# Kernel optimization log

Hardware: AMD Instinct MI355X
Metric: run time of the kernel (lower is better)

## Reference

```python
import jax, jax.numpy as jnp
import numpy as np

S, B, D, H, DH, E, F = 2048, 2, 512, 8, 64, 8, 1024
TOPK = 2


def setup_inputs() -> dict:
    key = jax.random.key(0)
    ks = jax.random.split(key, 12)
    rn = lambda k, shp, s=0.02: jax.random.normal(k, shp, jnp.float32) * s
    # RoPE tables (half-split convention): (S, DH)
    pos = jnp.arange(S, dtype=jnp.float32)[:, None]
    inv_freq = 1.0 / (10000.0 ** (jnp.arange(0, DH, 2, dtype=jnp.float32) / DH))
    ang = pos * inv_freq[None, :]                       # (S, DH//2)
    cos = jnp.concatenate([jnp.cos(ang), jnp.cos(ang)], axis=-1)
    sin = jnp.concatenate([jnp.sin(ang), jnp.sin(ang)], axis=-1)
    return {
        "src": jax.random.normal(ks[0], (S, B, D), jnp.float32),
        "cos": cos, "sin": sin,
        "Wq": rn(ks[1], (D, D)), "bq": jnp.zeros((D,), jnp.float32),
        "Wk": rn(ks[2], (D, D)), "bk": jnp.zeros((D,), jnp.float32),
        "Wv": rn(ks[3], (D, D)), "bv": jnp.zeros((D,), jnp.float32),
        "Wo": rn(ks[4], (D, D)), "bo": jnp.zeros((D,), jnp.float32),
        "ln1_g": jnp.ones((D,), jnp.float32), "ln1_b": jnp.zeros((D,), jnp.float32),
        "ln2_g": jnp.ones((D,), jnp.float32), "ln2_b": jnp.zeros((D,), jnp.float32),
        "Wg": rn(ks[5], (D, E)),
        "W1": rn(ks[6], (E, D, F)), "B1": jnp.zeros((E, F), jnp.float32),
        "W2": rn(ks[7], (E, F, D)), "B2": jnp.zeros((E, D), jnp.float32),
    }


def _layernorm(x, g, b, eps=1e-5):
    m = x.mean(-1, keepdims=True)
    v = ((x - m) ** 2).mean(-1, keepdims=True)
    return (x - m) * jax.lax.rsqrt(v + eps) * g + b


def _rotate_half(x):
    x1, x2 = jnp.split(x, 2, axis=-1)
    return jnp.concatenate([-x2, x1], axis=-1)


def _forward(src, cos, sin, Wq, bq, Wk, bk, Wv, bv, Wo, bo,
             ln1_g, ln1_b, ln2_g, ln2_b, Wg, W1, B1, W2, B2):
    # ---- RoPE self-attention ----
    q = (src @ Wq + bq).reshape(S, B, H, DH)
    k = (src @ Wk + bk).reshape(S, B, H, DH)
    v = (src @ Wv + bv).reshape(S, B, H, DH)
    c = cos[:, None, None, :]
    s = sin[:, None, None, :]
    q = q * c + _rotate_half(q) * s
    k = k * c + _rotate_half(k) * s
    scores = jnp.einsum("sbhd,tbhd->bhst", q, k) / jnp.sqrt(jnp.float32(DH))
    attn = jax.nn.softmax(scores, axis=-1)              # (B,H,S,S)
    ctx = jnp.einsum("bhst,tbhd->sbhd", attn, v).reshape(S, B, D)
    attn_out = ctx @ Wo + bo
    x = _layernorm(src + attn_out, ln1_g, ln1_b)
    # ---- MoE feed-forward (top-k softmax gating) ----
    xt = x.reshape(S * B, D)                            # (N, D)
    probs = jax.nn.softmax(xt @ Wg, axis=-1)            # (N, E)
    top_v, top_i = jax.lax.top_k(probs, TOPK)           # (N, TOPK)
    top_v = top_v / top_v.sum(-1, keepdims=True)
    N = S * B
    gates = jnp.zeros((N, E), jnp.float32).at[
        jnp.arange(N)[:, None], top_i].add(top_v)       # (N, E)
    h = jax.nn.relu(jnp.einsum("nd,edf->nef", xt, W1) + B1[None])   # (N,E,F)
    eo = jnp.einsum("nef,efd->ned", h, W2) + B2[None]               # (N,E,D)
    moe_out = jnp.einsum("ne,ned->nd", gates, eo).reshape(S, B, D)
    return _layernorm(x + moe_out, ln2_g, ln2_b)


def reference(src, cos, sin, Wq, bq, Wk, bk, Wv, bv, Wo, bo,
              ln1_g, ln1_b, ln2_g, ln2_b, Wg, W1, B1, W2, B2):
    return _forward(src, cos, sin, Wq, bq, Wk, bk, Wv, bv, Wo, bo,
                    ln1_g, ln1_b, ln2_g, ln2_b, Wg, W1, B1, W2, B2)
```

## Files before the change

kernel.cpp:

```cpp
#include <hip/hip_runtime.h>
#include <math.h>

#define S_  2048
#define B_  2
#define D_  512
#define H_  8
#define DH_ 64
#define E_  8
#define F_  1024
#define N_  4096
#define NPAIR_ 8192

typedef __attribute__((ext_vector_type(4))) float f32x4;
typedef __attribute__((ext_vector_type(8))) short short8;
typedef unsigned short u16;

__device__ __forceinline__ u16 f2bf(float f) {
  unsigned u = __builtin_bit_cast(unsigned, f);
  u += 0x7fffu + ((u >> 16) & 1u);
  return (u16)(u >> 16);
}
__device__ __forceinline__ float bf2f(u16 h) {
  unsigned u = ((unsigned)h) << 16;
  return __builtin_bit_cast(float, u);
}

__global__ __launch_bounds__(256) void src_split(const float* __restrict__ in,
                                                 u16* __restrict__ hi,
                                                 u16* __restrict__ lo) {
  size_t i = ((size_t)blockIdx.x * 256 + threadIdx.x) * 8;
  float f[8];
  *(float4*)&f[0] = *(const float4*)&in[i];
  *(float4*)&f[4] = *(const float4*)&in[i + 4];
  short8 h, l;
#pragma unroll
  for (int j = 0; j < 8; ++j) {
    u16 a = f2bf(f[j]);
    h[j] = (short)a;
    l[j] = (short)f2bf(f[j] - bf2f(a));
  }
  *(short8*)&hi[i] = h;
  *(short8*)&lo[i] = l;
}

__global__ __launch_bounds__(256) void wsplit_t(const float* __restrict__ W,
                                                u16* __restrict__ Whi,
                                                u16* __restrict__ Wlo,
                                                int Nn, int K) {
  __shared__ u16 Th[64][72];
  __shared__ u16 Tl[64][72];
  int kb = blockIdx.y * 64, nb = blockIdx.x * 64;
  int r = threadIdx.x >> 2, c0 = (threadIdx.x & 3) * 16;
  const float* wp = &W[(size_t)(kb + r) * Nn + nb + c0];
#pragma unroll
  for (int c = 0; c < 16; c += 4) {
    float4 t = *(const float4*)&wp[c];
    float f[4] = {t.x, t.y, t.z, t.w};
#pragma unroll
    for (int j = 0; j < 4; ++j) {
      u16 a = f2bf(f[j]);
      Th[r][c0 + c + j] = a;
      Tl[r][c0 + c + j] = f2bf(f[j] - bf2f(a));
    }
  }
  __syncthreads();
  short8 h0, h1, l0, l1;
#pragma unroll
  for (int j = 0; j < 8; ++j) {
    h0[j] = (short)Th[c0 + j][r];     h1[j] = (short)Th[c0 + 8 + j][r];
    l0[j] = (short)Tl[c0 + j][r];     l1[j] = (short)Tl[c0 + 8 + j][r];
  }
  size_t ob = (size_t)(nb + r) * K + kb + c0;
  *(short8*)&Whi[ob] = h0;  *(short8*)&Whi[ob + 8] = h1;
  *(short8*)&Wlo[ob] = l0;  *(short8*)&Wlo[ob + 8] = l1;
}

__global__ __launch_bounds__(256) void wtrans(const float* __restrict__ W,
                                              u16* __restrict__ Wt,
                                              int K, int Nn) {
  size_t eo = (size_t)blockIdx.z * K * Nn;
  __shared__ u16 T[64][72];
  int kb = blockIdx.y * 64, nb = blockIdx.x * 64;
  int r = threadIdx.x >> 2, c0 = (threadIdx.x & 3) * 16;
  const float* wp = &W[eo + (size_t)(kb + r) * Nn + nb + c0];
#pragma unroll
  for (int c = 0; c < 16; c += 4) {
    float4 t = *(const float4*)&wp[c];
    T[r][c0 + c + 0] = f2bf(t.x);
    T[r][c0 + c + 1] = f2bf(t.y);
    T[r][c0 + c + 2] = f2bf(t.z);
    T[r][c0 + c + 3] = f2bf(t.w);
  }
  __syncthreads();
  short8 s0, s1;
#pragma unroll
  for (int j = 0; j < 8; ++j) {
    s0[j] = (short)T[c0 + j][r];
    s1[j] = (short)T[c0 + 8 + j][r];
  }
  *(short8*)&Wt[eo + (size_t)(nb + r) * K + kb + c0] = s0;
  *(short8*)&Wt[eo + (size_t)(nb + r) * K + kb + c0 + 8] = s1;
}

__global__ __launch_bounds__(256) void qkv_mfma(const u16* __restrict__ Ah_g,
                                                const u16* __restrict__ Al_g,
                                                const u16* __restrict__ Bh_g,
                                                const u16* __restrict__ Bl_g,
                                                const float* __restrict__ bq,
                                                const float* __restrict__ bk,
                                                const float* __restrict__ bv,
                                                const float* __restrict__ cosb,
                                                const float* __restrict__ sinb,
                                                u16* __restrict__ qh, u16* __restrict__ ql,
                                                u16* __restrict__ kh, u16* __restrict__ kl,
                                                u16* __restrict__ vb) {
  __shared__ u16 Ah[128][40], Al[128][40], Bh[128][40], Bl[128][40];
  int tid = threadIdx.x;
  int w = tid >> 6, l = tid & 63;
  int wr = w >> 1, wc = w & 1;
  int lg = l >> 4, lx = l & 15;
  int m0 = blockIdx.x * 128, n0 = blockIdx.y * 128;
  int sr = tid >> 1, s16 = (tid & 1) * 16;
  const u16* Aph = Ah_g + (size_t)(m0 + sr) * 512;
  const u16* Apl = Al_g + (size_t)(m0 + sr) * 512;
  const u16* Bph = Bh_g + (size_t)(n0 + sr) * 512;
  const u16* Bpl = Bl_g + (size_t)(n0 + sr) * 512;
  f32x4 acc[4][4];
#pragma unroll
  for (int m = 0; m < 4; ++m)
#pragma unroll
    for (int n = 0; n < 4; ++n) acc[m][n] = (f32x4){0.f, 0.f, 0.f, 0.f};
  for (int k0 = 0; k0 < 512; k0 += 32) {
    short8 ah0 = *(const short8*)&Aph[k0 + s16];
    short8 ah1 = *(const short8*)&Aph[k0 + s16 + 8];
    short8 al0 = *(const short8*)&Apl[k0 + s16];
    short8 al1 = *(const short8*)&Apl[k0 + s16 + 8];
    short8 bh0 = *(const short8*)&Bph[k0 + s16];
    short8 bh1 = *(const short8*)&Bph[k0 + s16 + 8];
    short8 bl0 = *(const short8*)&Bpl[k0 + s16];
    short8 bl1 = *(const short8*)&Bpl[k0 + s16 + 8];
    __syncthreads();
    *(short8*)&Ah[sr][s16] = ah0; *(short8*)&Ah[sr][s16 + 8] = ah1;
    *(short8*)&Al[sr][s16] = al0; *(short8*)&Al[sr][s16 + 8] = al1;
    *(short8*)&Bh[sr][s16] = bh0; *(short8*)&Bh[sr][s16 + 8] = bh1;
    *(short8*)&Bl[sr][s16] = bl0; *(short8*)&Bl[sr][s16 + 8] = bl1;
    __syncthreads();
    short8 fah[4], fal[4], fbh[4], fbl[4];
#pragma unroll
    for (int m = 0; m < 4; ++m) {
      fah[m] = *(const short8*)&Ah[wr * 64 + m * 16 + lx][lg * 8];
      fal[m] = *(const short8*)&Al[wr * 64 + m * 16 + lx][lg * 8];
    }
#pragma unroll
    for (int n = 0; n < 4; ++n) {
      fbh[n] = *(const short8*)&Bh[wc * 64 + n * 16 + lx][lg * 8];
      fbl[n] = *(const short8*)&Bl[wc * 64 + n * 16 + lx][lg * 8];
    }
#pragma unroll
    for (int m = 0; m < 4; ++m)
#pragma unroll
      for (int n = 0; n < 4; ++n) {
        acc[m][n] = __builtin_amdgcn_mfma_f32_16x16x32_bf16(fah[m], fbh[n], acc[m][n], 0, 0, 0);
        acc[m][n] = __builtin_amdgcn_mfma_f32_16x16x32_bf16(fal[m], fbh[n], acc[m][n], 0, 0, 0);
        acc[m][n] = __builtin_amdgcn_mfma_f32_16x16x32_bf16(fah[m], fbl[n], acc[m][n], 0, 0, 0);
      }
  }
  int tcolbase = n0 + wc * 64;
  int tsel = tcolbase >> 9;
  int hbase = tcolbase & 511;
  const float* bias = (tsel == 0) ? bq : (tsel == 1) ? bk : bv;
  if (tsel == 2) {
#pragma unroll
    for (int m = 0; m < 4; ++m)
#pragma unroll
      for (int i = 0; i < 4; ++i) {
        int row = m0 + wr * 64 + m * 16 + lg * 4 + i;
#pragma unroll
        for (int n = 0; n < 4; ++n) {
          int col = hbase + n * 16 + lx;
          vb[(size_t)row * 512 + col] = f2bf(acc[m][n][i] + bias[col]);
        }
      }
  } else {
    u16* oh = tsel ? kh : qh;
    u16* ol = tsel ? kl : ql;
    float qsc = tsel ? 1.f : 0.125f;
#pragma unroll
    for (int m = 0; m < 4; ++m)
#pragma unroll
      for (int i = 0; i < 4; ++i) {
        int row = m0 + wr * 64 + m * 16 + lg * 4 + i;
        int s = row >> 1;
#pragma unroll
        for (int n = 0; n < 2; ++n) {
          int dln = n * 16 + lx;
          float c  = cosb[s * 64 + dln];
          float sn = sinb[s * 64 + dln];
          float a  = acc[m][n][i]     + bias[hbase + dln];
          float b2 = acc[m][n + 2][i] + bias[hbase + dln + 32];
          float ra = (a * c - b2 * sn) * qsc;
          float rb = (b2 * c + a * sn) * qsc;
          size_t ix = (size_t)row * 512 + hbase + dln;
          u16 rah = f2bf(ra);
          oh[ix] = rah; ol[ix] = f2bf(ra - bf2f(rah));
          u16 rbh = f2bf(rb);
          oh[ix + 32] = rbh; ol[ix + 32] = f2bf(rb - bf2f(rbh));
        }
      }
  }
}

__global__ __launch_bounds__(256) void attn_mfma2(const u16* __restrict__ qh,
                                                  const u16* __restrict__ ql,
                                                  const u16* __restrict__ kh,
                                                  const u16* __restrict__ kl,
                                                  const u16* __restrict__ vbuf,
                                                  u16* __restrict__ poh,
                                                  u16* __restrict__ pol,
                                                  float* __restrict__ pml) {
  __shared__ u16 Khi[64][72];
  __shared__ u16 Klo[64][72];
  __shared__ u16 Vt[64][72];
  __shared__ u16 Pl[4][16][72];
  int tid = threadIdx.x;
  int w = tid >> 6, l = tid & 63;
  int lg = l >> 4, lx = l & 15;
  int f = blockIdx.x;
  int xcd = f & 7, j = f >> 3;
  int slab = xcd + 8 * (j & 3);
  int qt = j >> 2;
  int bh = slab >> 1, kvh = slab & 1;
  int b = bh >> 3, h = bh & 7;

  short8 qfh[2], qfl[2];
  {
    int qrow = qt * 64 + w * 16 + lx;
    size_t qo = (size_t)(qrow * 2 + b) * 512 + h * 64 + lg * 8;
    qfh[0] = *(const short8*)&qh[qo];
    qfh[1] = *(const short8*)&qh[qo + 32];
    qfl[0] = *(const short8*)&ql[qo];
    qfl[1] = *(const short8*)&ql[qo + 32];
  }

  f32x4 o_acc[4];
#pragma unroll
  for (int dg = 0; dg < 4; ++dg) o_acc[dg] = (f32x4){0.f, 0.f, 0.f, 0.f};
  float m_run[4], l_run[4];
#pragma unroll
  for (int i = 0; i < 4; ++i) { m_run[i] = -1e30f; l_run[i] = 0.f; }

  int kvr = tid >> 2, ds4 = (tid & 3) * 16;
  int kvc = tid & 63, dsg = (tid >> 6) * 16;

  for (int tt = 0; tt < 1024; tt += 64) {
    int t0 = kvh * 1024 + tt;
    __syncthreads();
    {
      size_t ko = (size_t)((t0 + kvr) * 2 + b) * 512 + h * 64 + ds4;
      *(short8*)&Khi[kvr][ds4]     = *(const short8*)&kh[ko];
      *(short8*)&Khi[kvr][ds4 + 8] = *(const short8*)&kh[ko + 8];
      *(short8*)&Klo[kvr][ds4]     = *(const short8*)&kl[ko];
      *(short8*)&Klo[kvr][ds4 + 8] = *(const short8*)&kl[ko + 8];
      size_t vo = (size_t)((t0 + kvc) * 2 + b) * 512 + h * 64 + dsg;
      short8 v0 = *(const short8*)&vbuf[vo];
      short8 v1 = *(const short8*)&vbuf[vo + 8];
#pragma unroll
      for (int c = 0; c < 8; ++c) {
        Vt[dsg + c][kvc] = (u16)v0[c];
        Vt[dsg + 8 + c][kvc] = (u16)v1[c];
      }
    }
    __syncthreads();

    f32x4 sc[4];
#pragma unroll
    for (int cg = 0; cg < 4; ++cg) {
      short8 kh0 = *(const short8*)&Khi[cg * 16 + lx][lg * 8];
      short8 kh1 = *(const short8*)&Khi[cg * 16 + lx][32 + lg * 8];
      short8 kl0 = *(const short8*)&Klo[cg * 16 + lx][lg * 8];
      short8 kl1 = *(const short8*)&Klo[cg * 16 + lx][32 + lg * 8];
      f32x4 a = (f32x4){0.f, 0.f, 0.f, 0.f};
      a = __builtin_amdgcn_mfma_f32_16x16x32_bf16(qfh[0], kh0, a, 0, 0, 0);
      a = __builtin_amdgcn_mfma_f32_16x16x32_bf16(qfh[1], kh1, a, 0, 0, 0);
      a = __builtin_amdgcn_mfma_f32_16x16x32_bf16(qfl[0], kh0, a, 0, 0, 0);
      a = __builtin_amdgcn_mfma_f32_16x16x32_bf16(qfl[1], kh1, a, 0, 0, 0);
      a = __builtin_amdgcn_mfma_f32_16x16x32_bf16(qfh[0], kl0, a, 0, 0, 0);
      a = __builtin_amdgcn_mfma_f32_16x16x32_bf16(qfh[1], kl1, a, 0, 0, 0);
      sc[cg] = a;
    }

#pragma unroll
    for (int i = 0; i < 4; ++i) {
      float s0 = sc[0][i], s1 = sc[1][i], s2 = sc[2][i], s3 = sc[3][i];
      float tm = fmaxf(fmaxf(s0, s1), fmaxf(s2, s3));
      tm = fmaxf(tm, __shfl_xor(tm, 1));
      tm = fmaxf(tm, __shfl_xor(tm, 2));
      tm = fmaxf(tm, __shfl_xor(tm, 4));
      tm = fmaxf(tm, __shfl_xor(tm, 8));
      float mn = fmaxf(m_run[i], tm);
      float corr = __expf(m_run[i] - mn);
      m_run[i] = mn;
      float p0 = __expf(s0 - mn), p1 = __expf(s1 - mn);
      float p2 = __expf(s2 - mn), p3 = __expf(s3 - mn);
      float ts = p0 + p1 + p2 + p3;
      ts += __shfl_xor(ts, 1); ts += __shfl_xor(ts, 2);
      ts += __shfl_xor(ts, 4); ts += __shfl_xor(ts, 8);
      l_run[i] = l_run[i] * corr + ts;
#pragma unroll
      for (int dg = 0; dg < 4; ++dg) o_acc[dg][i] *= corr;
      int row = lg * 4 + i;
      Pl[w][row][lx]      = f2bf(p0);
      Pl[w][row][16 + lx] = f2bf(p1);
      Pl[w][row][32 + lx] = f2bf(p2);
      Pl[w][row][48 + lx] = f2bf(p3);
    }

    short8 pa0 = *(const short8*)&Pl[w][lx][lg * 8];
    short8 pa1 = *(const short8*)&Pl[w][lx][32 + lg * 8];
#pragma unroll
    for (int dg = 0; dg < 4; ++dg) {
      short8 v0 = *(const short8*)&Vt[dg * 16 + lx][lg * 8];
      short8 v1 = *(const short8*)&Vt[dg * 16 + lx][32 + lg * 8];
      o_acc[dg] = __builtin_amdgcn_mfma_f32_16x16x32_bf16(pa0, v0, o_acc[dg], 0, 0, 0);
      o_acc[dg] = __builtin_amdgcn_mfma_f32_16x16x32_bf16(pa1, v1, o_acc[dg], 0, 0, 0);
    }
  }

#pragma unroll
  for (int i = 0; i < 4; ++i) {
    int srow = qt * 64 + w * 16 + lg * 4 + i;
    int row2 = srow * 2 + b;
    size_t base = (size_t)kvh * ((size_t)N_ * D_) + (size_t)row2 * 512 + h * 64;
#pragma unroll
    for (int dg = 0; dg < 4; ++dg) {
      float val = o_acc[dg][i];
      u16 hi = f2bf(val);
      poh[base + dg * 16 + lx] = hi;
      pol[base + dg * 16 + lx] = f2bf(val - bf2f(hi));
    }
    if (lx == 0) {
      int u = row2 * 8 + h;
      pml[(size_t)kvh * 65536 + u * 2 + 0] = m_run[i];
      pml[(size_t)kvh * 65536 + u * 2 + 1] = l_run[i];
    }
  }
}

__global__ __launch_bounds__(256) void merge_attn2(const u16* __restrict__ poh,
                                                   const u16* __restrict__ pol,
                                                   const float* __restrict__ pml,
                                                   u16* __restrict__ ch,
                                                   u16* __restrict__ cl) {
  int u = blockIdx.x * 4 + (threadIdx.x >> 6);
  int lane = threadIdx.x & 63;
  float m0 = pml[u * 2], l0 = pml[u * 2 + 1];
  float m1 = pml[65536 + u * 2], l1 = pml[65536 + u * 2 + 1];
  float m = fmaxf(m0, m1);
  float e0 = __expf(m0 - m), e1 = __expf(m1 - m);
  float inv = 1.f / (l0 * e0 + l1 * e1);
  int n = u >> 3, h = u & 7;
  size_t base = (size_t)n * 512 + h * 64 + lane;
  const size_t PO1 = (size_t)N_ * D_;
  float v0 = bf2f(poh[base]) + bf2f(pol[base]);
  float v1 = bf2f(poh[PO1 + base]) + bf2f(pol[PO1 + base]);
  float val = (v0 * e0 + v1 * e1) * inv;
  u16 hi = f2bf(val);
  ch[base] = hi;
  cl[base] = f2bf(val - bf2f(hi));
}

__global__ __launch_bounds__(256) void wo_mfma(const u16* __restrict__ Ah_g,
                                               const u16* __restrict__ Al_g,
                                               const u16* __restrict__ Bh_g,
                                               const u16* __restrict__ Bl_g,
                                               const float* __restrict__ bias,
                                               float* __restrict__ C) {
  __shared__ u16 Ah[128][40], Al[128][40], Bh[128][40], Bl[128][40];
  int tid = threadIdx.x;
  int w = tid >> 6, l = tid & 63;
  int wr = w >> 1, wc = w & 1;
  int lg = l >> 4, lx = l & 15;
  int m0 = blockIdx.x * 128, n0 = blockIdx.y * 128;
  int sr = tid >> 1, s16 = (tid & 1) * 16;
  const u16* Aph = Ah_g + (size_t)(m0 + sr) * 512;
  const u16* Apl = Al_g + (size_t)(m0 + sr) * 512;
  const u16* Bph = Bh_g + (size_t)(n0 + sr) * 512;
  const u16* Bpl = Bl_g + (size_t)(n0 + sr) * 512;
  f32x4 acc[4][4];
#pragma unroll
  for (int m = 0; m < 4; ++m)
#pragma unroll
    for (int n = 0; n < 4; ++n) acc[m][n] = (f32x4){0.f, 0.f, 0.f, 0.f};
  for (int k0 = 0; k0 < 512; k0 += 32) {
    short8 ah0 = *(const short8*)&Aph[k0 + s16];
    short8 ah1 = *(const short8*)&Aph[k0 + s16 + 8];
    short8 al0 = *(const short8*)&Apl[k0 + s16];
    short8 al1 = *(const short8*)&Apl[k0 + s16 + 8];
    short8 bh0 = *(const short8*)&Bph[k0 + s16];
    short8 bh1 = *(const short8*)&Bph[k0 + s16 + 8];
    short8 bl0 = *(const short8*)&Bpl[k0 + s16];
    short8 bl1 = *(const short8*)&Bpl[k0 + s16 + 8];
    __syncthreads();
    *(short8*)&Ah[sr][s16] = ah0; *(short8*)&Ah[sr][s16 + 8] = ah1;
    *(short8*)&Al[sr][s16] = al0; *(short8*)&Al[sr][s16 + 8] = al1;
    *(short8*)&Bh[sr][s16] = bh0; *(short8*)&Bh[sr][s16 + 8] = bh1;
    *(short8*)&Bl[sr][s16] = bl0; *(short8*)&Bl[sr][s16 + 8] = bl1;
    __syncthreads();
    short8 fah[4], fal[4], fbh[4], fbl[4];
#pragma unroll
    for (int m = 0; m < 4; ++m) {
      fah[m] = *(const short8*)&Ah[wr * 64 + m * 16 + lx][lg * 8];
      fal[m] = *(const short8*)&Al[wr * 64 + m * 16 + lx][lg * 8];
    }
#pragma unroll
    for (int n = 0; n < 4; ++n) {
      fbh[n] = *(const short8*)&Bh[wc * 64 + n * 16 + lx][lg * 8];
      fbl[n] = *(const short8*)&Bl[wc * 64 + n * 16 + lx][lg * 8];
    }
#pragma unroll
    for (int m = 0; m < 4; ++m)
#pragma unroll
      for (int n = 0; n < 4; ++n) {
        acc[m][n] = __builtin_amdgcn_mfma_f32_16x16x32_bf16(fah[m], fbh[n], acc[m][n], 0, 0, 0);
        acc[m][n] = __builtin_amdgcn_mfma_f32_16x16x32_bf16(fal[m], fbh[n], acc[m][n], 0, 0, 0);
        acc[m][n] = __builtin_amdgcn_mfma_f32_16x16x32_bf16(fah[m], fbl[n], acc[m][n], 0, 0, 0);
      }
  }
#pragma unroll
  for (int m = 0; m < 4; ++m)
#pragma unroll
    for (int i = 0; i < 4; ++i) {
      int row = m0 + wr * 64 + m * 16 + lg * 4 + i;
#pragma unroll
      for (int n = 0; n < 4; ++n) {
        int col = n0 + wc * 64 + n * 16 + lx;
        C[(size_t)row * 512 + col] = acc[m][n][i] + bias[col];
      }
    }
}

__global__ __launch_bounds__(256) void ln_res(const float* __restrict__ a,
                                              const float* __restrict__ b,
                                              const float* __restrict__ g,
                                              const float* __restrict__ beta,
                                              float* __restrict__ out,
                                              u16* __restrict__ obf) {
  int n = blockIdx.x * 4 + (threadIdx.x >> 6);
  int lane = threadIdx.x & 63;
  float v[8];
  float s = 0.f;
#pragma unroll
  for (int i = 0; i < 8; ++i) {
    int d = lane + 64 * i;
    v[i] = a[(size_t)n * D_ + d] + b[(size_t)n * D_ + d];
    s += v[i];
  }
#pragma unroll
  for (int m = 32; m; m >>= 1) s += __shfl_xor(s, m);
  float mean = s * (1.f / D_);
  float s2 = 0.f;
#pragma unroll
  for (int i = 0; i < 8; ++i) { float t = v[i] - mean; s2 += t * t; }
#pragma unroll
  for (int m = 32; m; m >>= 1) s2 += __shfl_xor(s2, m);
  float r = rsqrtf(s2 * (1.f / D_) + 1e-5f);
#pragma unroll
  for (int i = 0; i < 8; ++i) {
    int d = lane + 64 * i;
    float val = (v[i] - mean) * r * g[d] + beta[d];
    out[(size_t)n * D_ + d] = val;
    obf[(size_t)n * D_ + d] = f2bf(val);
  }
}

__global__ __launch_bounds__(256) void ln2_final(const float* __restrict__ x,
                                                 const u16* __restrict__ mp,
                                                 const float* __restrict__ g,
                                                 const float* __restrict__ beta,
                                                 float* __restrict__ out) {
  int n = blockIdx.x * 4 + (threadIdx.x >> 6);
  int lane = threadIdx.x & 63;
  float v[8];
  float s = 0.f;
#pragma unroll
  for (int i = 0; i < 8; ++i) {
    int d = lane + 64 * i;
    v[i] = x[(size_t)n * D_ + d] + bf2f(mp[(size_t)(2 * n) * D_ + d]) +
           bf2f(mp[(size_t)(2 * n + 1) * D_ + d]);
    s += v[i];
  }
#pragma unroll
  for (int m = 32; m; m >>= 1) s += __shfl_xor(s, m);
  float mean = s * (1.f / D_);
  float s2 = 0.f;
#pragma unroll
  for (int i = 0; i < 8; ++i) { float t = v[i] - mean; s2 += t * t; }
#pragma unroll
  for (int m = 32; m; m >>= 1) s2 += __shfl_xor(s2, m);
  float r = rsqrtf(s2 * (1.f / D_) + 1e-5f);
#pragma unroll
  for (int i = 0; i < 8; ++i) {
    int d = lane + 64 * i;
    out[(size_t)n * D_ + d] = (v[i] - mean) * r * g[d] + beta[d];
  }
}

__global__ __launch_bounds__(256) void gate_compute(const float* __restrict__ x,
                                                    const float* __restrict__ Wg,
                                                    float* __restrict__ gp,
                                                    int* __restrict__ tope) {
  int n = blockIdx.x * 4 + (threadIdx.x >> 6);
  int lane = threadIdx.x & 63;
  float p[E_] = {};
  for (int d = lane; d < D_; d += 64) {
    float xv = x[(size_t)n * D_ + d];
    const float* wr = &Wg[(size_t)d * E_];
#pragma unroll
    for (int e = 0; e < E_; ++e) p[e] += xv * wr[e];
  }
#pragma unroll
  for (int e = 0; e < E_; ++e)
#pragma unroll
    for (int m = 32; m; m >>= 1) p[e] += __shfl_xor(p[e], m);
  if (lane == 0) {
    float mx = p[0];
#pragma unroll
    for (int e = 1; e < E_; ++e) mx = fmaxf(mx, p[e]);
    float q[E_];
#pragma unroll
    for (int e = 0; e < E_; ++e) q[e] = expf(p[e] - mx);
    int e1 = 0;
#pragma unroll
    for (int e = 1; e < E_; ++e) if (q[e] > q[e1]) e1 = e;
    int e2 = (e1 == 0) ? 1 : 0;
#pragma unroll
    for (int e = 0; e < E_; ++e) if (e != e1 && q[e] > q[e2]) e2 = e;
    float denom = q[e1] + q[e2];
    gp[n * 2] = q[e1] / denom;
    gp[n * 2 + 1] = q[e2] / denom;
    tope[n] = e1 | (e2 << 8);
  }
}

__global__ __launch_bounds__(256) void route_build(const int* __restrict__ tope,
                                                   int* __restrict__ cnt,
                                                   int* __restrict__ lst) {
  int e = blockIdx.x;
  __shared__ int wsum[4];
  __shared__ int basem;
  int tid = threadIdx.x;
  int w = tid >> 6, lane = tid & 63;
  if (tid == 0) basem = 0;
  __syncthreads();
  for (int c0 = 0; c0 < N_; c0 += 256) {
    int n = c0 + tid;
    int te = tope[n];
    int e1 = te & 0xff, e2 = (te >> 8) & 0xff;
    bool m2 = (e2 == e);
    bool flag = (e1 == e) || m2;
    unsigned long long mask = __ballot(flag);
    int wpre = __popcll(mask & ((1ull << lane) - 1ull));
    if (lane == 0) wsum[w] = __popcll(mask);
    __syncthreads();
    int woff = 0;
    for (int i = 0; i < w; ++i) woff += wsum[i];
    int total = wsum[0] + wsum[1] + wsum[2] + wsum[3];
    if (flag) lst[e * N_ + basem + woff + wpre] = n * 2 + (m2 ? 1 : 0);
    __syncthreads();
    if (tid == 0) basem += total;
    __syncthreads();
  }
  if (tid == 0) cnt[e] = basem;
}

template <int MODE>
__global__ __launch_bounds__(256) void moe_mfma(const u16* __restrict__ Abase,
                                                const u16* __restrict__ Wt,
                                                const float* __restrict__ bias,
                                                const float* __restrict__ gp,
                                                u16* __restrict__ outp,
                                                const int* __restrict__ cnt,
                                                const int* __restrict__ lst) {
  constexpr int K  = MODE ? 1024 : 512;
  constexpr int Nn = MODE ? 512 : 1024;
  constexpr int NT = Nn / 128;
  constexpr int NI = K / 32;
  int fidx = blockIdx.x;
  int e = fidx & 7;
  int r = fidx >> 3;
  int nt = r % NT;
  int mt = r / NT;
  int c = cnt[e];
  int m0 = mt * 64;
  if (m0 >= c) return;
  int off = 0;
#pragma unroll
  for (int i = 0; i < E_; ++i) if (i < e) off += cnt[i];
  int n0 = nt * 128;
  __shared__ u16 As[64][40];
  __shared__ u16 Bs[128][40];
  int tid = threadIdx.x;
  int w = tid >> 6, l = tid & 63;
  int lg = l >> 4, lx = l & 15;
  int arow = tid >> 2, aseg = (tid & 3) * 8;
  int brow = tid >> 1, bseg = (tid & 1) * 16;
  int ar = m0 + arow; if (ar >= c) ar = c - 1;
  const u16* Ap;
  if (MODE == 0) Ap = Abase + (size_t)(lst[e * N_ + ar] >> 1) * 512 + aseg;
  else           Ap = Abase + (size_t)(off + ar) * 1024 + aseg;
  const u16* Bp = Wt + (size_t)e * K * Nn + (size_t)(n0 + brow) * K + bseg;

  f32x4 acc[4][2];
#pragma unroll
  for (int m = 0; m < 4; ++m)
#pragma unroll
    for (int n = 0; n < 2; ++n) acc[m][n] = (f32x4){0.f, 0.f, 0.f, 0.f};

  short8 pa  = *(const short8*)&Ap[0];
  short8 pb0 = *(const short8*)&Bp[0];
  short8 pb1 = *(const short8*)&Bp[8];
  for (int kk = 0; kk < NI; ++kk) {
    __syncthreads();
    *(short8*)&As[arow][aseg] = pa;
    *(short8*)&Bs[brow][bseg] = pb0;
    *(short8*)&Bs[brow][bseg + 8] = pb1;
    __syncthreads();
    if (kk + 1 < NI) {
      int ko = (kk + 1) * 32;
      pa  = *(const short8*)&Ap[ko];
      pb0 = *(const short8*)&Bp[ko];
      pb1 = *(const short8*)&Bp[ko + 8];
    }
    short8 af[4], bf[2];
#pragma unroll
    for (int m = 0; m < 4; ++m)
      af[m] = *(const short8*)&As[m * 16 + lx][lg * 8];
#pragma unroll
    for (int n = 0; n < 2; ++n)
      bf[n] = *(const short8*)&Bs[w * 32 + n * 16 + lx][lg * 8];
#pragma unroll
    for (int m = 0; m < 4; ++m)
#pragma unroll
      for (int n = 0; n < 2; ++n)
        acc[m][n] = __builtin_amdgcn_mfma_f32_16x16x32_bf16(af[m], bf[n], acc[m][n], 0, 0, 0);
  }
#pragma unroll
  for (int m = 0; m < 4; ++m)
#pragma unroll
    for (int i = 0; i < 4; ++i) {
      int rr = m0 + m * 16 + lg * 4 + i;
      if (rr < c) {
#pragma unroll
        for (int n = 0; n < 2; ++n) {
          int col = n0 + w * 32 + n * 16 + lx;
          float val = acc[m][n][i] + bias[e * Nn + col];
          if (MODE == 0) {
            outp[(size_t)(off + rr) * 1024 + col] = f2bf(fmaxf(val, 0.f));
          } else {
            int p = lst[e * N_ + rr];
            outp[(size_t)p * 512 + col] = f2bf(gp[p] * val);
          }
        }
      }
    }
}

extern "C" void kernel_launch(void* const* d_in, const int* in_sizes, int n_in,
                              void* d_out, int out_size, void* d_ws, size_t ws_size,
                              hipStream_t stream) {
  const float* src  = (const float*)d_in[0];
  const float* cosb = (const float*)d_in[1];
  const float* sinb = (const float*)d_in[2];
  const float* Wq   = (const float*)d_in[3];
  const float* bq   = (const float*)d_in[4];
  const float* Wk   = (const float*)d_in[5];
  const float* bk   = (const float*)d_in[6];
  const float* Wv   = (const float*)d_in[7];
  const float* bv   = (const float*)d_in[8];
  const float* Wo   = (const float*)d_in[9];
  const float* bo   = (const float*)d_in[10];
  const float* ln1g = (const float*)d_in[11];
  const float* ln1b = (const float*)d_in[12];
  const float* ln2g = (const float*)d_in[13];
  const float* ln2b = (const float*)d_in[14];
  const float* Wg   = (const float*)d_in[15];
  const float* W1   = (const float*)d_in[16];
  const float* B1   = (const float*)d_in[17];
  const float* W2   = (const float*)d_in[18];
  const float* B2   = (const float*)d_in[19];
  float* out = (float*)d_out;
  char* wsb = (char*)d_ws;

  const size_t MB1 = 1u << 20;
  u16* sh   = (u16*)(wsb + 0 * MB1);
  u16* sl   = (u16*)(wsb + 4 * MB1);
  u16* qhb  = (u16*)(wsb + 8 * MB1);
  u16* qlb  = (u16*)(wsb + 12 * MB1);
  u16* khb  = (u16*)(wsb + 16 * MB1);
  u16* klb  = (u16*)(wsb + 20 * MB1);
  u16* vbuf = (u16*)(wsb + 24 * MB1);
  u16* poh  = (u16*)(wsb + 28 * MB1);
  u16* pol  = (u16*)(wsb + 36 * MB1);
  float* pml = (float*)(wsb + 44 * MB1);
  float* aob = (float*)(wsb + 28 * MB1);
  float* xb  = (float*)(wsb + 36 * MB1);
  u16* xbf   = (u16*)(wsb + 44 * MB1);
  u16* Wqkv_hi = (u16*)(wsb + 48 * MB1);
  u16* Wqkv_lo = (u16*)(wsb + 48 * MB1 + 1572864);
  u16* Wo_hi   = (u16*)(wsb + 48 * MB1 + 3145728);
  u16* Wo_lo   = (u16*)(wsb + 48 * MB1 + 3670016);
  u16* W1t     = (u16*)(wsb + 52 * MB1);
  u16* W2t     = (u16*)(wsb + 28 * MB1);
  float* gpb   = (float*)(wsb + 60 * MB1);
  int* cnt     = (int*)(wsb + 60 * MB1 + 32768);
  int* lst     = (int*)(wsb + 60 * MB1 + 32768 + 64);
  int* tope    = (int*)(wsb + 60 * MB1 + 32768 + 64 + 131072);
  u16* ch  = sh;
  u16* cl  = sl;
  u16* hbf = (u16*)(wsb + 8 * MB1);
  u16* mp  = (u16*)(wsb + 0 * MB1);

  dim3 blk(256);
  src_split<<<dim3(1024), blk, 0, stream>>>(src, sh, sl);
  wsplit_t<<<dim3(8, 8), blk, 0, stream>>>(Wq, Wqkv_hi, Wqkv_lo, 512, 512);
  wsplit_t<<<dim3(8, 8), blk, 0, stream>>>(Wk, Wqkv_hi + 512 * 512, Wqkv_lo + 512 * 512, 512, 512);
  wsplit_t<<<dim3(8, 8), blk, 0, stream>>>(Wv, Wqkv_hi + 1024 * 512, Wqkv_lo + 1024 * 512, 512, 512);
  wsplit_t<<<dim3(8, 8), blk, 0, stream>>>(Wo, Wo_hi, Wo_lo, 512, 512);
  qkv_mfma<<<dim3(32, 12), blk, 0, stream>>>(sh, sl, Wqkv_hi, Wqkv_lo, bq, bk, bv,
                                             cosb, sinb, qhb, qlb, khb, klb, vbuf);
  attn_mfma2<<<dim3(1024), blk, 0, stream>>>(qhb, qlb, khb, klb, vbuf, poh, pol, pml);
  merge_attn2<<<dim3(8192), blk, 0, stream>>>(poh, pol, pml, ch, cl);
  wo_mfma<<<dim3(32, 4), blk, 0, stream>>>(ch, cl, Wo_hi, Wo_lo, bo, aob);
  ln_res<<<dim3(1024), blk, 0, stream>>>(src, aob, ln1g, ln1b, xb, xbf);
  wtrans<<<dim3(8, 16, 8), blk, 0, stream>>>(W2, W2t, 1024, 512);
  wtrans<<<dim3(16, 8, 8), blk, 0, stream>>>(W1, W1t, 512, 1024);
  gate_compute<<<dim3(1024), blk, 0, stream>>>(xb, Wg, gpb, tope);
  route_build<<<dim3(8), blk, 0, stream>>>(tope, cnt, lst);
  moe_mfma<0><<<dim3(8 * 8 * 64), blk, 0, stream>>>(xbf, W1t, B1, gpb, hbf, cnt, lst);
  moe_mfma<1><<<dim3(8 * 4 * 64), blk, 0, stream>>>(hbf, W2t, B2, gpb, mp, cnt, lst);
  ln2_final<<<dim3(1024), blk, 0, stream>>>(xb, mp, ln2g, ln2b, out);
}
```

Before: 253.5 us.

## Prefetch next K-tile into registers in GEMMs and attention, swizzle P buffer

The QKV GEMM, the output GEMM and the flash-attention loop now load the next K/V or A/B tile from global memory into registers right after the LDS store barrier. This lets the global-load latency overlap with the MFMA work on the current tile. The attention P scratch buffer also gets an XOR swizzle on the column index to cut LDS bank conflicts between the P writes and the pa0/pa1 reads. The cost is higher register pressure from the prefetch registers, which could lower occupancy.

```diff
diff --git a/kernel.cpp b/kernel.cpp
--- a/kernel.cpp
+++ b/kernel.cpp
@@ -130,21 +130,28 @@
   for (int m = 0; m < 4; ++m)
 #pragma unroll
     for (int n = 0; n < 4; ++n) acc[m][n] = (f32x4){0.f, 0.f, 0.f, 0.f};
+  short8 ah0 = *(const short8*)&Aph[s16];
+  short8 ah1 = *(const short8*)&Aph[s16 + 8];
+  short8 al0 = *(const short8*)&Apl[s16];
+  short8 al1 = *(const short8*)&Apl[s16 + 8];
+  short8 bh0 = *(const short8*)&Bph[s16];
+  short8 bh1 = *(const short8*)&Bph[s16 + 8];
+  short8 bl0 = *(const short8*)&Bpl[s16];
+  short8 bl1 = *(const short8*)&Bpl[s16 + 8];
   for (int k0 = 0; k0 < 512; k0 += 32) {
-    short8 ah0 = *(const short8*)&Aph[k0 + s16];
-    short8 ah1 = *(const short8*)&Aph[k0 + s16 + 8];
-    short8 al0 = *(const short8*)&Apl[k0 + s16];
-    short8 al1 = *(const short8*)&Apl[k0 + s16 + 8];
-    short8 bh0 = *(const short8*)&Bph[k0 + s16];
-    short8 bh1 = *(const short8*)&Bph[k0 + s16 + 8];
-    short8 bl0 = *(const short8*)&Bpl[k0 + s16];
-    short8 bl1 = *(const short8*)&Bpl[k0 + s16 + 8];
     __syncthreads();
     *(short8*)&Ah[sr][s16] = ah0; *(short8*)&Ah[sr][s16 + 8] = ah1;
     *(short8*)&Al[sr][s16] = al0; *(short8*)&Al[sr][s16 + 8] = al1;
     *(short8*)&Bh[sr][s16] = bh0; *(short8*)&Bh[sr][s16 + 8] = bh1;
     *(short8*)&Bl[sr][s16] = bl0; *(short8*)&Bl[sr][s16 + 8] = bl1;
     __syncthreads();
+    if (k0 + 32 < 512) {
+      int ko = k0 + 32 + s16;
+      ah0 = *(const short8*)&Aph[ko]; ah1 = *(const short8*)&Aph[ko + 8];
+      al0 = *(const short8*)&Apl[ko]; al1 = *(const short8*)&Apl[ko + 8];
+      bh0 = *(const short8*)&Bph[ko]; bh1 = *(const short8*)&Bph[ko + 8];
+      bl0 = *(const short8*)&Bpl[ko]; bl1 = *(const short8*)&Bpl[ko + 8];
+    }
     short8 fah[4], fal[4], fbh[4], fbl[4];
 #pragma unroll
     for (int m = 0; m < 4; ++m) {
@@ -251,41 +258,53 @@
 
   int kvr = tid >> 2, ds4 = (tid & 3) * 16;
   int kvc = tid & 63, dsg = (tid >> 6) * 16;
+  int psw = ((lx >> 2) & 3) << 3;
+
+  short8 rkh0, rkh1, rkl0, rkl1, rv0, rv1;
+  {
+    int t0 = kvh * 1024;
+    size_t ko = (size_t)((t0 + kvr) * 2 + b) * 512 + h * 64 + ds4;
+    rkh0 = *(const short8*)&kh[ko]; rkh1 = *(const short8*)&kh[ko + 8];
+    rkl0 = *(const short8*)&kl[ko]; rkl1 = *(const short8*)&kl[ko + 8];
+    size_t vo = (size_t)((t0 + kvc) * 2 + b) * 512 + h * 64 + dsg;
+    rv0 = *(const short8*)&vbuf[vo]; rv1 = *(const short8*)&vbuf[vo + 8];
+  }
 
   for (int tt = 0; tt < 1024; tt += 64) {
-    int t0 = kvh * 1024 + tt;
-    __syncthreads();
-    {
+    __syncthreads();
+    *(short8*)&Khi[kvr][ds4]     = rkh0;
+    *(short8*)&Khi[kvr][ds4 + 8] = rkh1;
+    *(short8*)&Klo[kvr][ds4]     = rkl0;
+    *(short8*)&Klo[kvr][ds4 + 8] = rkl1;
+#pragma unroll
+    for (int c = 0; c < 8; ++c) {
+      Vt[dsg + c][kvc] = (u16)rv0[c];
+      Vt[dsg + 8 + c][kvc] = (u16)rv1[c];
+    }
+    __syncthreads();
+    if (tt + 64 < 1024) {
+      int t0 = kvh * 1024 + tt + 64;
       size_t ko = (size_t)((t0 + kvr) * 2 + b) * 512 + h * 64 + ds4;
-      *(short8*)&Khi[kvr][ds4]     = *(const short8*)&kh[ko];
-      *(short8*)&Khi[kvr][ds4 + 8] = *(const short8*)&kh[ko + 8];
-      *(short8*)&Klo[kvr][ds4]     = *(const short8*)&kl[ko];
-      *(short8*)&Klo[kvr][ds4 + 8] = *(const short8*)&kl[ko + 8];
+      rkh0 = *(const short8*)&kh[ko]; rkh1 = *(const short8*)&kh[ko + 8];
+      rkl0 = *(const short8*)&kl[ko]; rkl1 = *(const short8*)&kl[ko + 8];
       size_t vo = (size_t)((t0 + kvc) * 2 + b) * 512 + h * 64 + dsg;
-      short8 v0 = *(const short8*)&vbuf[vo];
-      short8 v1 = *(const short8*)&vbuf[vo + 8];
-#pragma unroll
-      for (int c = 0; c < 8; ++c) {
-        Vt[dsg + c][kvc] = (u16)v0[c];
-        Vt[dsg + 8 + c][kvc] = (u16)v1[c];
-      }
-    }
-    __syncthreads();
+      rv0 = *(const short8*)&vbuf[vo]; rv1 = *(const short8*)&vbuf[vo + 8];
+    }
 
     f32x4 sc[4];
 #pragma unroll
     for (int cg = 0; cg < 4; ++cg) {
-      short8 kh0 = *(const short8*)&Khi[cg * 16 + lx][lg * 8];
-      short8 kh1 = *(const short8*)&Khi[cg * 16 + lx][32 + lg * 8];
-      short8 kl0 = *(const short8*)&Klo[cg * 16 + lx][lg * 8];
-      short8 kl1 = *(const short8*)&Klo[cg * 16 + lx][32 + lg * 8];
+      short8 kf0 = *(const short8*)&Khi[cg * 16 + lx][lg * 8];
+      short8 kf1 = *(const short8*)&Khi[cg * 16 + lx][32 + lg * 8];
+      short8 kg0 = *(const short8*)&Klo[cg * 16 + lx][lg * 8];
+      short8 kg1 = *(const short8*)&Klo[cg * 16 + lx][32 + lg * 8];
       f32x4 a = (f32x4){0.f, 0.f, 0.f, 0.f};
-      a = __builtin_amdgcn_mfma_f32_16x16x32_bf16(qfh[0], kh0, a, 0, 0, 0);
-      a = __builtin_amdgcn_mfma_f32_16x16x32_bf16(qfh[1], kh1, a, 0, 0, 0);
-      a = __builtin_amdgcn_mfma_f32_16x16x32_bf16(qfl[0], kh0, a, 0, 0, 0);
-      a = __builtin_amdgcn_mfma_f32_16x16x32_bf16(qfl[1], kh1, a, 0, 0, 0);
-      a = __builtin_amdgcn_mfma_f32_16x16x32_bf16(qfh[0], kl0, a, 0, 0, 0);
-      a = __builtin_amdgcn_mfma_f32_16x16x32_bf16(qfh[1], kl1, a, 0, 0, 0);
+      a = __builtin_amdgcn_mfma_f32_16x16x32_bf16(qfh[0], kf0, a, 0, 0, 0);
+      a = __builtin_amdgcn_mfma_f32_16x16x32_bf16(qfh[1], kf1, a, 0, 0, 0);
+      a = __builtin_amdgcn_mfma_f32_16x16x32_bf16(qfl[0], kf0, a, 0, 0, 0);
+      a = __builtin_amdgcn_mfma_f32_16x16x32_bf16(qfl[1], kf1, a, 0, 0, 0);
+      a = __builtin_amdgcn_mfma_f32_16x16x32_bf16(qfh[0], kg0, a, 0, 0, 0);
+      a = __builtin_amdgcn_mfma_f32_16x16x32_bf16(qfh[1], kg1, a, 0, 0, 0);
       sc[cg] = a;
     }
 
@@ -309,14 +328,15 @@
 #pragma unroll
       for (int dg = 0; dg < 4; ++dg) o_acc[dg][i] *= corr;
       int row = lg * 4 + i;
-      Pl[w][row][lx]      = f2bf(p0);
-      Pl[w][row][16 + lx] = f2bf(p1);
-      Pl[w][row][32 + lx] = f2bf(p2);
-      Pl[w][row][48 + lx] = f2bf(p3);
-    }
-
-    short8 pa0 = *(const short8*)&Pl[w][lx][lg * 8];
-    short8 pa1 = *(const short8*)&Pl[w][lx][32 + lg * 8];
+      int sw = ((row >> 2) & 3) << 3;
+      Pl[w][row][lx ^ sw]        = f2bf(p0);
+      Pl[w][row][(16 + lx) ^ sw] = f2bf(p1);
+      Pl[w][row][(32 + lx) ^ sw] = f2bf(p2);
+      Pl[w][row][(48 + lx) ^ sw] = f2bf(p3);
+    }
+
+    short8 pa0 = *(const short8*)&Pl[w][lx][(lg * 8) ^ psw];
+    short8 pa1 = *(const short8*)&Pl[w][lx][(32 + lg * 8) ^ psw];
 #pragma unroll
     for (int dg = 0; dg < 4; ++dg) {
       short8 v0 = *(const short8*)&Vt[dg * 16 + lx][lg * 8];
@@ -391,21 +411,28 @@
   for (int m = 0; m < 4; ++m)
 #pragma unroll
     for (int n = 0; n < 4; ++n) acc[m][n] = (f32x4){0.f, 0.f, 0.f, 0.f};
+  short8 ah0 = *(const short8*)&Aph[s16];
+  short8 ah1 = *(const short8*)&Aph[s16 + 8];
+  short8 al0 = *(const short8*)&Apl[s16];
+  short8 al1 = *(const short8*)&Apl[s16 + 8];
+  short8 bh0 = *(const short8*)&Bph[s16];
+  short8 bh1 = *(const short8*)&Bph[s16 + 8];
+  short8 bl0 = *(const short8*)&Bpl[s16];
+  short8 bl1 = *(const short8*)&Bpl[s16 + 8];
   for (int k0 = 0; k0 < 512; k0 += 32) {
-    short8 ah0 = *(const short8*)&Aph[k0 + s16];
-    short8 ah1 = *(const short8*)&Aph[k0 + s16 + 8];
-    short8 al0 = *(const short8*)&Apl[k0 + s16];
-    short8 al1 = *(const short8*)&Apl[k0 + s16 + 8];
-    short8 bh0 = *(const short8*)&Bph[k0 + s16];
-    short8 bh1 = *(const short8*)&Bph[k0 + s16 + 8];
-    short8 bl0 = *(const short8*)&Bpl[k0 + s16];
-    short8 bl1 = *(const short8*)&Bpl[k0 + s16 + 8];
     __syncthreads();
     *(short8*)&Ah[sr][s16] = ah0; *(short8*)&Ah[sr][s16 + 8] = ah1;
     *(short8*)&Al[sr][s16] = al0; *(short8*)&Al[sr][s16 + 8] = al1;
     *(short8*)&Bh[sr][s16] = bh0; *(short8*)&Bh[sr][s16 + 8] = bh1;
     *(short8*)&Bl[sr][s16] = bl0; *(short8*)&Bl[sr][s16 + 8] = bl1;
     __syncthreads();
+    if (k0 + 32 < 512) {
+      int ko = k0 + 32 + s16;
+      ah0 = *(const short8*)&Aph[ko]; ah1 = *(const short8*)&Aph[ko + 8];
+      al0 = *(const short8*)&Apl[ko]; al1 = *(const short8*)&Apl[ko + 8];
+      bh0 = *(const short8*)&Bph[ko]; bh1 = *(const short8*)&Bph[ko + 8];
+      bl0 = *(const short8*)&Bpl[ko]; bl1 = *(const short8*)&Bpl[ko + 8];
+    }
     short8 fah[4], fal[4], fbh[4], fbl[4];
 #pragma unroll
     for (int m = 0; m < 4; ++m) {
```

Measured after the change: 251.1 us. About the same (-1.0%).
